# Optimization experiments

Hardware: AMD Instinct MI355X
Metric: run time of the kernel (lower is better)

Reference implementation:

```python
import jax, jax.numpy as jnp
import numpy as np

B, S, D_IN, HID, H = 4, 2048, 1024, 1024, 16
DH = HID // H


def setup_inputs() -> dict:
    key = jax.random.key(0)
    ks = jax.random.split(key, 10)
    s = 0.02
    return {
        "x": jax.random.normal(ks[0], (B, S, D_IN), dtype=jnp.float32),
        "Wq": jax.random.normal(ks[1], (D_IN, HID), dtype=jnp.float32) * s,
        "bq": jnp.zeros((HID,), dtype=jnp.float32),
        "Wk": jax.random.normal(ks[2], (D_IN, HID), dtype=jnp.float32) * s,
        "bk": jnp.zeros((HID,), dtype=jnp.float32),
        "Wv": jax.random.normal(ks[3], (D_IN, HID), dtype=jnp.float32) * s,
        "bv": jnp.zeros((HID,), dtype=jnp.float32),
        "Wo": jax.random.normal(ks[4], (HID, HID), dtype=jnp.float32) * s,
        "bo": jnp.zeros((HID,), dtype=jnp.float32),
        "padding_mask": jax.random.randint(ks[5], (B, S), 0, 2, dtype=jnp.int32),
    }


def reference(x, Wq, bq, Wk, bk, Wv, bv, Wo, bo, padding_mask):
    b, s, _ = x.shape
    q = (x @ Wq + bq).reshape(b, s, H, DH)  # [b, s, h, dh]
    k = (x @ Wk + bk).reshape(b, s, H, DH)
    v = (x @ Wv + bv).reshape(b, s, H, DH)

    # ALiBi: symmetric |i-j| distance bias, per-head slopes 2^{-m}
    r = jnp.arange(s)
    pos = jnp.abs(r[None, :] - r[:, None]).astype(jnp.float32)  # [s, s]
    step = 8.0 / H
    slopes = jnp.power(2.0, -jnp.arange(step, 8.0 + step, step, dtype=jnp.float32))  # [h]
    alibi = slopes[:, None, None] * pos[None, :, :]  # [h, s, s]

    scale = jnp.sqrt(jnp.float32(DH))
    attn = jnp.einsum("bqhd,bkhd->bhqk", q, k)
    attn = (attn - alibi[None]) / scale
    attn = jnp.where(padding_mask[:, None, None, :] == 0, -jnp.inf, attn)
    p = jax.nn.softmax(attn, axis=-1)

    out = jnp.einsum("bhqk,bkhd->bqhd", p, v).reshape(b, s, HID)
    return out @ Wo + bo
```

## Files before the change

kernel.cpp:

```cpp
#include <hip/hip_runtime.h>
#include <stdint.h>

#define NB     4
#define SEQ    2048
#define NH     16
#define DHD    64
#define DM     1024
#define MTOT   (NB*SEQ)
#define HSZ    (SEQ*DHD)

typedef __attribute__((ext_vector_type(8))) short bf16x8;
typedef __attribute__((ext_vector_type(4))) float f32x4;

__device__ __forceinline__ short f2bf(float f) {
  uint32_t u = __float_as_uint(f);
  u = (u + 0x7FFFu + ((u >> 16) & 1u)) >> 16;
  return (short)u;
}

__device__ __forceinline__ uint32_t cvtpk(float lo, float hi) {
  uint32_t r;
  asm("v_cvt_pk_bf16_f32 %0, %1, %2" : "=v"(r) : "v"(lo), "v"(hi));
  return r;
}

__device__ __forceinline__ float exp2a(float x) {
  float r;
  asm("v_exp_f32 %0, %1" : "=v"(r) : "v"(x));
  return r;
}

__device__ __forceinline__ float max3f(float a, float b, float c) {
  return fmaxf(fmaxf(a, b), c);
}

__device__ __forceinline__ f32x4 mfma16(bf16x8 a, bf16x8 b, f32x4 c) {
  return __builtin_amdgcn_mfma_f32_16x16x32_bf16(a, b, c, 0, 0, 0);
}

__device__ __forceinline__ void async16(const void* g, void* l) {
  __builtin_amdgcn_global_load_lds(
      (const __attribute__((address_space(1))) void*)g,
      (__attribute__((address_space(3))) void*)l, 16, 0, 0);
}

__global__ void k_cast(const float* __restrict__ in, short* __restrict__ out, int n) {
  int i = (blockIdx.x * blockDim.x + threadIdx.x) * 8;
  if (i >= n) return;
  float4 a = *reinterpret_cast<const float4*>(in + i);
  float4 b = *reinterpret_cast<const float4*>(in + i + 4);
  bf16x8 v;
  v[0] = f2bf(a.x); v[1] = f2bf(a.y); v[2] = f2bf(a.z); v[3] = f2bf(a.w);
  v[4] = f2bf(b.x); v[5] = f2bf(b.y); v[6] = f2bf(b.z); v[7] = f2bf(b.w);
  *reinterpret_cast<bf16x8*>(out + i) = v;
}

__global__ void k_maskbias(const int* __restrict__ pm, float* __restrict__ fb, int n) {
  int i = blockIdx.x * blockDim.x + threadIdx.x;
  if (i < n) fb[i] = pm[i] ? 0.0f : -1e30f;
}

__global__ void k_transpose4(const float* __restrict__ Wq, const float* __restrict__ Wk,
                             const float* __restrict__ Wv, const float* __restrict__ Wo,
                             short* __restrict__ wqkv, short* __restrict__ wot) {
  __shared__ float tile[32][33];
  int z = blockIdx.z;
  const float* in = (z == 0) ? Wq : (z == 1) ? Wk : (z == 2) ? Wv : Wo;
  short* out = (z < 3) ? (wqkv + (size_t)z * 1024 * DM) : wot;
  int n0 = blockIdx.x * 32, k0 = blockIdx.y * 32;
  int tx = threadIdx.x, ty = threadIdx.y;
  #pragma unroll
  for (int i = 0; i < 32; i += 8)
    tile[ty + i][tx] = in[(size_t)(k0 + ty + i) * DM + n0 + tx];
  __syncthreads();
  #pragma unroll
  for (int i = 0; i < 32; i += 8)
    out[(size_t)(n0 + ty + i) * DM + k0 + tx] = f2bf(tile[tx][ty + i]);
}

__global__ void __launch_bounds__(256) k_gemm_qkv(const short* __restrict__ A,
                                                  const short* __restrict__ Bt,
                                                  const float* __restrict__ bq,
                                                  const float* __restrict__ bk,
                                                  const float* __restrict__ bv,
                                                  short* __restrict__ Qo,
                                                  short* __restrict__ KF,
                                                  short* __restrict__ VF,
                                                  float qscale) {
  __shared__ short lA[128 * 32];
  __shared__ short lB[128 * 32];
  int lin = blockIdx.y * gridDim.x + blockIdx.x;
  int swz = (lin & 7) * 192 + (lin >> 3);
  int m0 = (swz & 63) * 128, n0 = (swz >> 6) * 128;
  int seg = n0 >> 10;
  const float* bias = (seg == 0) ? bq : (seg == 1) ? bk : bv;
  float scale = (seg == 0) ? qscale : 1.0f;
  int tid = threadIdx.x, lane = tid & 63, w = tid >> 6;
  int wr = w >> 1, wc = w & 1;
  int l15 = lane & 15, lg = lane >> 4;
  f32x4 acc[4][4] = {};

  int r0 = tid >> 2, c0 = (tid & 3) * 8;
  int r1 = (tid + 256) >> 2, c1 = ((tid + 256) & 3) * 8;
  const short* ga0 = A + (size_t)(m0 + r0) * DM + c0;
  const short* ga1 = A + (size_t)(m0 + r1) * DM + c1;
  const short* gb0 = Bt + (size_t)(n0 + r0) * DM + c0;
  const short* gb1 = Bt + (size_t)(n0 + r1) * DM + c1;
  short* lA0 = lA + w * 512;
  short* lA1 = lA + 2048 + w * 512;
  short* lB0 = lB + w * 512;
  short* lB1 = lB + 2048 + w * 512;

  for (int k0 = 0; k0 < DM; k0 += 32) {
    async16(ga0 + k0, lA0);
    async16(ga1 + k0, lA1);
    async16(gb0 + k0, lB0);
    async16(gb1 + k0, lB1);
    __syncthreads();
    bf16x8 af[4], bfr[4];
    #pragma unroll
    for (int i = 0; i < 4; ++i) {
      af[i]  = *reinterpret_cast<const bf16x8*>(lA + (wr * 64 + i * 16 + l15) * 32 + lg * 8);
      bfr[i] = *reinterpret_cast<const bf16x8*>(lB + (wc * 64 + i * 16 + l15) * 32 + lg * 8);
    }
    #pragma unroll
    for (int i = 0; i < 4; ++i)
      #pragma unroll
      for (int j = 0; j < 4; ++j)
        acc[i][j] = mfma16(af[i], bfr[j], acc[i][j]);
    __syncthreads();
  }

  #pragma unroll
  for (int j = 0; j < 4; ++j) {
    int cg = n0 + wc * 64 + j * 16 + l15;
    int cloc = cg & 1023;
    float bval = bias[cloc];
    #pragma unroll
    for (int i = 0; i < 4; ++i) {
      #pragma unroll
      for (int r = 0; r < 4; ++r) {
        int rg = m0 + wr * 64 + i * 16 + lg * 4 + r;
        float val = (acc[i][j][r] + bval) * scale;
        if (seg == 0) {
          Qo[(size_t)rg * DM + cloc] = f2bf(val);
        } else if (seg == 1) {
          int bh2 = ((rg >> 11) << 4) | (cloc >> 6);
          int dh = cloc & 63, sl = rg & 2047;
          size_t fi = (size_t)bh2 * HSZ + (size_t)(sl >> 4) * 1024
                    + (size_t)((((dh >> 3) * 16 + (sl & 15)) * 8) + (dh & 7));
          KF[fi] = f2bf(val);
        } else {
          int bh2 = ((rg >> 11) << 4) | (cloc >> 6);
          int dh = cloc & 63, sl = rg & 2047;
          size_t fi = (size_t)bh2 * HSZ + (size_t)(sl >> 6) * 4096
                    + (size_t)((((dh >> 4) * 8 + ((sl >> 3) & 7)) * 16 + (dh & 15)) * 8 + (sl & 7));
          VF[fi] = f2bf(val);
        }
      }
    }
  }
}

__global__ void __launch_bounds__(256) k_gemm_out(const short* __restrict__ A,
                                                  const short* __restrict__ Bt,
                                                  const float* __restrict__ bias,
                                                  float* __restrict__ C) {
  __shared__ short lA[128 * 32];
  __shared__ short lB[128 * 32];
  int lin = blockIdx.y * gridDim.x + blockIdx.x;
  int s = ((lin & 7) << 6) | (lin >> 3);
  int m0 = (s & 63) * 128, n0 = (s >> 6) * 128;
  int tid = threadIdx.x, lane = tid & 63, w = tid >> 6;
  int wr = w >> 1, wc = w & 1;
  int l15 = lane & 15, lg = lane >> 4;
  f32x4 acc[4][4] = {};

  int r0 = tid >> 2, c0 = (tid & 3) * 8;
  int r1 = (tid + 256) >> 2, c1 = ((tid + 256) & 3) * 8;
  const short* ga0 = A + (size_t)(m0 + r0) * DM + c0;
  const short* ga1 = A + (size_t)(m0 + r1) * DM + c1;
  const short* gb0 = Bt + (size_t)(n0 + r0) * DM + c0;
  const short* gb1 = Bt + (size_t)(n0 + r1) * DM + c1;
  short* lA0 = lA + w * 512;
  short* lA1 = lA + 2048 + w * 512;
  short* lB0 = lB + w * 512;
  short* lB1 = lB + 2048 + w * 512;

  for (int k0 = 0; k0 < DM; k0 += 32) {
    async16(ga0 + k0, lA0);
    async16(ga1 + k0, lA1);
    async16(gb0 + k0, lB0);
    async16(gb1 + k0, lB1);
    __syncthreads();
    bf16x8 af[4], bfr[4];
    #pragma unroll
    for (int i = 0; i < 4; ++i) {
      af[i]  = *reinterpret_cast<const bf16x8*>(lA + (wr * 64 + i * 16 + l15) * 32 + lg * 8);
      bfr[i] = *reinterpret_cast<const bf16x8*>(lB + (wc * 64 + i * 16 + l15) * 32 + lg * 8);
    }
    #pragma unroll
    for (int i = 0; i < 4; ++i)
      #pragma unroll
      for (int j = 0; j < 4; ++j)
        acc[i][j] = mfma16(af[i], bfr[j], acc[i][j]);
    __syncthreads();
  }

  #pragma unroll
  for (int j = 0; j < 4; ++j) {
    int cg = n0 + wc * 64 + j * 16 + l15;
    float bv = bias[cg];
    #pragma unroll
    for (int i = 0; i < 4; ++i) {
      #pragma unroll
      for (int r = 0; r < 4; ++r) {
        int rg = m0 + wr * 64 + i * 16 + lg * 4 + r;
        C[(size_t)rg * DM + cg] = acc[i][j][r] + bv;
      }
    }
  }
}

__device__ __forceinline__ void softmax_half(const f32x4* st, const float4* fb4,
                                             float c2, float d0, int lg,
                                             float& mrun, float& ssum,
                                             f32x4* acc, uint32_t* wb) {
  float l[16];
  #pragma unroll
  for (int t = 0; t < 4; ++t) {
    l[t * 4 + 0] = fmaf(-c2, fabsf(d0 - (float)(t * 16 + 0)), st[t][0] + fb4[t].x);
    l[t * 4 + 1] = fmaf(-c2, fabsf(d0 - (float)(t * 16 + 1)), st[t][1] + fb4[t].y);
    l[t * 4 + 2] = fmaf(-c2, fabsf(d0 - (float)(t * 16 + 2)), st[t][2] + fb4[t].z);
    l[t * 4 + 3] = fmaf(-c2, fabsf(d0 - (float)(t * 16 + 3)), st[t][3] + fb4[t].w);
  }
  float ma = max3f(l[0], l[1], l[2]);
  float mb = max3f(l[3], l[4], l[5]);
  float mc = max3f(l[6], l[7], l[8]);
  float md = max3f(l[9], l[10], l[11]);
  float me = max3f(l[12], l[13], l[14]);
  float tmax = fmaxf(max3f(ma, mb, mc), max3f(md, me, l[15]));

  if (!__all(tmax <= mrun + 8.0f)) {
    tmax = fmaxf(tmax, __shfl_xor(tmax, 16));
    tmax = fmaxf(tmax, __shfl_xor(tmax, 32));
    float mn = fmaxf(mrun, tmax);
    float fsc = exp2a(mrun - mn);
    mrun = mn;
    ssum *= fsc;
    #pragma unroll
    for (int td = 0; td < 4; ++td) acc[td] *= fsc;
  }

  float p[16];
  #pragma unroll
  for (int i = 0; i < 16; ++i) p[i] = exp2a(l[i] - mrun);
  float a0 = p[0] + p[1],  a1 = p[2] + p[3],  a2 = p[4] + p[5],  a3 = p[6] + p[7];
  float a4 = p[8] + p[9],  a5 = p[10] + p[11], a6 = p[12] + p[13], a7 = p[14] + p[15];
  float b0 = a0 + a1, b1 = a2 + a3, b2 = a4 + a5, b3 = a6 + a7;
  ssum += (b0 + b1) + (b2 + b3);

  #pragma unroll
  for (int t = 0; t < 4; ++t) {
    uint2 wv = { cvtpk(p[t * 4 + 0], p[t * 4 + 1]), cvtpk(p[t * 4 + 2], p[t * 4 + 3]) };
    *reinterpret_cast<uint2*>(wb + t * 8 + lg * 2) = wv;
  }
}

#define ISSUE_KA(DST, KT) do {                                              \
  const short* kp_ = kbase + (size_t)((KT) >> 4) * 1024;                    \
  _Pragma("unroll")                                                         \
  for (int t_ = 0; t_ < 4; ++t_) {                                          \
    DST[t_][0] = *reinterpret_cast<const bf16x8*>(kp_ + t_ * 1024);         \
    DST[t_][1] = *reinterpret_cast<const bf16x8*>(kp_ + t_ * 1024 + 512);   \
  }                                                                         \
} while (0)

#define TILE(KA, KAN, KT, PRE) do {                                         \
  float4 fb4[4];                                                            \
  _Pragma("unroll")                                                         \
  for (int t_ = 0; t_ < 4; ++t_)                                            \
    fb4[t_] = *reinterpret_cast<const float4*>(fb + (KT) + t_ * 16 + lg * 4);\
  const short* vp_ = vbase + (size_t)((KT) >> 6) * 4096;                    \
  bf16x8 va[4][2];                                                          \
  _Pragma("unroll")                                                         \
  for (int td_ = 0; td_ < 4; ++td_) {                                       \
    va[td_][0] = *reinterpret_cast<const bf16x8*>(vp_ + (td_ * 8 + 0) * 128);\
    va[td_][1] = *reinterpret_cast<const bf16x8*>(vp_ + (td_ * 8 + 4) * 128);\
  }                                                                         \
  if (PRE) { ISSUE_KA(KAN, (KT) + 64); }                                    \
  __builtin_amdgcn_sched_barrier(0);                                        \
  f32x4 stA[4], stB[4];                                                     \
  __builtin_amdgcn_s_setprio(1);                                            \
  _Pragma("unroll")                                                         \
  for (int t_ = 0; t_ < 4; ++t_) {                                          \
    f32x4 zA = {};                                                          \
    zA = mfma16(KA[t_][0], bqA0, zA);                                       \
    stA[t_] = mfma16(KA[t_][1], bqA1, zA);                                  \
    f32x4 zB = {};                                                          \
    zB = mfma16(KA[t_][0], bqB0, zB);                                       \
    stB[t_] = mfma16(KA[t_][1], bqB1, zB);                                  \
  }                                                                         \
  __builtin_amdgcn_s_setprio(0);                                            \
  softmax_half(stA, fb4, c2, d0A, lg, mrunA, ssumA, accA, wbA);             \
  softmax_half(stB, fb4, c2, d0B, lg, mrunB, ssumB, accB, wbB);             \
  asm volatile("s_waitcnt lgkmcnt(0)" ::: "memory");                        \
  __builtin_amdgcn_sched_barrier(0);                                        \
  __builtin_amdgcn_s_setprio(1);                                            \
  _Pragma("unroll")                                                         \
  for (int ks_ = 0; ks_ < 2; ++ks_) {                                       \
    int t_ = ks_ * 2 + (lg >> 1);                                           \
    bf16x8 pfA = *reinterpret_cast<const bf16x8*>(wbA + t_ * 8 + (lg & 1) * 4);\
    bf16x8 pfB = *reinterpret_cast<const bf16x8*>(wbB + t_ * 8 + (lg & 1) * 4);\
    _Pragma("unroll")                                                       \
    for (int td_ = 0; td_ < 4; ++td_) {                                     \
      accA[td_] = mfma16(va[td_][ks_], pfA, accA[td_]);                     \
      accB[td_] = mfma16(va[td_][ks_], pfB, accB[td_]);                     \
    }                                                                       \
  }                                                                         \
  __builtin_amdgcn_s_setprio(0);                                            \
  d0A -= 64.0f; d0B -= 64.0f;                                               \
} while (0)

__global__ void __launch_bounds__(64, 2) k_attn(const short* __restrict__ Q,
                                                const short* __restrict__ KF,
                                                const short* __restrict__ VF,
                                                const float* __restrict__ fbias,
                                                short* __restrict__ O) {
  __shared__ uint32_t pbuf[2 * 16 * 38];
  int g = blockIdx.x;
  int qb = (g >> 3) & 63;
  int bh = (g & 7) + ((g >> 9) << 3);
  int b = bh >> 4, h = bh & 15;
  int lane = threadIdx.x;
  int l15 = lane & 15, lg = lane >> 4;
  int q0 = qb * 32;
  float c2 = exp2f(-0.5f * (float)(h + 1)) * 0.125f * 1.44269504f;

  const short* qpA = Q + (size_t)(b * SEQ + q0 + l15) * DM + h * DHD + lg * 8;
  bf16x8 bqA0 = *reinterpret_cast<const bf16x8*>(qpA);
  bf16x8 bqA1 = *reinterpret_cast<const bf16x8*>(qpA + 32);
  const short* qpB = qpA + (size_t)16 * DM;
  bf16x8 bqB0 = *reinterpret_cast<const bf16x8*>(qpB);
  bf16x8 bqB1 = *reinterpret_cast<const bf16x8*>(qpB + 32);

  const short* kbase = KF + (size_t)bh * HSZ + lane * 8;
  const short* vbase = VF + (size_t)bh * HSZ + lane * 8;
  const float* fb = fbias + b * SEQ;
  uint32_t* wbA = pbuf + l15 * 38;
  uint32_t* wbB = pbuf + 608 + l15 * 38;

  float mrunA = 0.0f, ssumA = 0.0f, mrunB = 0.0f, ssumB = 0.0f;
  f32x4 accA[4] = {}, accB[4] = {};
  float d0A = (float)(q0 + l15) - (float)(lg * 4);
  float d0B = d0A + 16.0f;

  bf16x8 kaX[4][2], kaY[4][2];
  ISSUE_KA(kaX, 0);

  for (int kt = 0; kt < SEQ; kt += 128) {
    TILE(kaX, kaY, kt, true);
    TILE(kaY, kaX, kt + 64, (kt + 128) < SEQ);
  }

  ssumA += __shfl_xor(ssumA, 16);
  ssumA += __shfl_xor(ssumA, 32);
  ssumB += __shfl_xor(ssumB, 16);
  ssumB += __shfl_xor(ssumB, 32);

  float invA = 1.0f / ssumA;
  float invB = 1.0f / ssumB;
  short* opA = O + (size_t)(b * SEQ + q0 + l15) * DM + h * DHD;
  short* opB = opA + (size_t)16 * DM;
  #pragma unroll
  for (int td = 0; td < 4; ++td) {
    uint2 wvA = { cvtpk(accA[td][0] * invA, accA[td][1] * invA),
                  cvtpk(accA[td][2] * invA, accA[td][3] * invA) };
    *reinterpret_cast<uint2*>(opA + td * 16 + lg * 4) = wvA;
    uint2 wvB = { cvtpk(accB[td][0] * invB, accB[td][1] * invB),
                  cvtpk(accB[td][2] * invB, accB[td][3] * invB) };
    *reinterpret_cast<uint2*>(opB + td * 16 + lg * 4) = wvB;
  }
}

extern "C" void kernel_launch(void* const* d_in, const int* in_sizes, int n_in,
                              void* d_out, int out_size, void* d_ws, size_t ws_size,
                              hipStream_t stream) {
  const float* x  = (const float*)d_in[0];
  const float* Wq = (const float*)d_in[1];
  const float* bq = (const float*)d_in[2];
  const float* Wk = (const float*)d_in[3];
  const float* bk = (const float*)d_in[4];
  const float* Wv = (const float*)d_in[5];
  const float* bv = (const float*)d_in[6];
  const float* Wo = (const float*)d_in[7];
  const float* bo = (const float*)d_in[8];
  const int*   pm = (const int*)d_in[9];

  char* ws = (char*)d_ws;
  const size_t MB = 1ull << 20;
  short* xb   = (short*)(ws + 0 * MB);
  short* q    = (short*)(ws + 16 * MB);
  short* kf   = (short*)(ws + 32 * MB);
  short* vf   = (short*)(ws + 48 * MB);
  short* ob   = (short*)(ws + 64 * MB);
  short* wqkv = (short*)(ws + 80 * MB);
  short* wot  = (short*)(ws + 86 * MB);
  float* fbias = (float*)(ws + 88 * MB);

  k_cast<<<dim3(MTOT * DM / 8 / 256), dim3(256), 0, stream>>>(x, xb, MTOT * DM);
  k_maskbias<<<dim3(MTOT / 256), dim3(256), 0, stream>>>(pm, fbias, MTOT);
  k_transpose4<<<dim3(32, 32, 4), dim3(32, 8), 0, stream>>>(Wq, Wk, Wv, Wo, wqkv, wot);
  k_gemm_qkv<<<dim3(64, 24), dim3(256), 0, stream>>>(xb, wqkv, bq, bk, bv,
                                                     q, kf, vf, 0.125f * 1.44269504f);
  k_attn<<<dim3(SEQ / 32 * NB * NH), dim3(64), 0, stream>>>(q, kf, vf, fbias, ob);
  k_gemm_out<<<dim3(64, 8), dim3(256), 0, stream>>>(ob, wot, bo, (float*)d_out);
}
```

Measured before the change: 238.3 us.

## Software-pipeline attention PV matmul one tile behind softmax with double-buffered P and V

The P·V MFMA for each key tile is deferred to the next tile's iteration. It now overlaps with the next QK^T and softmax instead of waiting on the LDS writes of P right after they are issued. P is double-buffered in shared memory and V fragments are double-buffered in registers. When a running-max rescale is needed, the pending PV is flushed first so it uses the old scale, and a final PV drains the pipeline after the loop. This costs extra VGPRs and twice the LDS for P, which may pressure occupancy.

```diff
diff --git a/kernel.cpp b/kernel.cpp
--- a/kernel.cpp
+++ b/kernel.cpp
@@ -222,51 +222,6 @@
   }
 }
 
-__device__ __forceinline__ void softmax_half(const f32x4* st, const float4* fb4,
-                                             float c2, float d0, int lg,
-                                             float& mrun, float& ssum,
-                                             f32x4* acc, uint32_t* wb) {
-  float l[16];
-  #pragma unroll
-  for (int t = 0; t < 4; ++t) {
-    l[t * 4 + 0] = fmaf(-c2, fabsf(d0 - (float)(t * 16 + 0)), st[t][0] + fb4[t].x);
-    l[t * 4 + 1] = fmaf(-c2, fabsf(d0 - (float)(t * 16 + 1)), st[t][1] + fb4[t].y);
-    l[t * 4 + 2] = fmaf(-c2, fabsf(d0 - (float)(t * 16 + 2)), st[t][2] + fb4[t].z);
-    l[t * 4 + 3] = fmaf(-c2, fabsf(d0 - (float)(t * 16 + 3)), st[t][3] + fb4[t].w);
-  }
-  float ma = max3f(l[0], l[1], l[2]);
-  float mb = max3f(l[3], l[4], l[5]);
-  float mc = max3f(l[6], l[7], l[8]);
-  float md = max3f(l[9], l[10], l[11]);
-  float me = max3f(l[12], l[13], l[14]);
-  float tmax = fmaxf(max3f(ma, mb, mc), max3f(md, me, l[15]));
-
-  if (!__all(tmax <= mrun + 8.0f)) {
-    tmax = fmaxf(tmax, __shfl_xor(tmax, 16));
-    tmax = fmaxf(tmax, __shfl_xor(tmax, 32));
-    float mn = fmaxf(mrun, tmax);
-    float fsc = exp2a(mrun - mn);
-    mrun = mn;
-    ssum *= fsc;
-    #pragma unroll
-    for (int td = 0; td < 4; ++td) acc[td] *= fsc;
-  }
-
-  float p[16];
-  #pragma unroll
-  for (int i = 0; i < 16; ++i) p[i] = exp2a(l[i] - mrun);
-  float a0 = p[0] + p[1],  a1 = p[2] + p[3],  a2 = p[4] + p[5],  a3 = p[6] + p[7];
-  float a4 = p[8] + p[9],  a5 = p[10] + p[11], a6 = p[12] + p[13], a7 = p[14] + p[15];
-  float b0 = a0 + a1, b1 = a2 + a3, b2 = a4 + a5, b3 = a6 + a7;
-  ssum += (b0 + b1) + (b2 + b3);
-
-  #pragma unroll
-  for (int t = 0; t < 4; ++t) {
-    uint2 wv = { cvtpk(p[t * 4 + 0], p[t * 4 + 1]), cvtpk(p[t * 4 + 2], p[t * 4 + 3]) };
-    *reinterpret_cast<uint2*>(wb + t * 8 + lg * 2) = wv;
-  }
-}
-
 #define ISSUE_KA(DST, KT) do {                                              \
   const short* kp_ = kbase + (size_t)((KT) >> 4) * 1024;                    \
   _Pragma("unroll")                                                         \
@@ -276,17 +231,70 @@
   }                                                                         \
 } while (0)
 
-#define TILE(KA, KAN, KT, PRE) do {                                         \
+#define LOGITS(ST, FB4, D0, L, TMX) do {                                    \
+  _Pragma("unroll")                                                         \
+  for (int t_ = 0; t_ < 4; ++t_) {                                          \
+    L[t_ * 4 + 0] = fmaf(-c2, fabsf((D0) - (float)(t_ * 16 + 0)), ST[t_][0] + FB4[t_].x); \
+    L[t_ * 4 + 1] = fmaf(-c2, fabsf((D0) - (float)(t_ * 16 + 1)), ST[t_][1] + FB4[t_].y); \
+    L[t_ * 4 + 2] = fmaf(-c2, fabsf((D0) - (float)(t_ * 16 + 2)), ST[t_][2] + FB4[t_].z); \
+    L[t_ * 4 + 3] = fmaf(-c2, fabsf((D0) - (float)(t_ * 16 + 3)), ST[t_][3] + FB4[t_].w); \
+  }                                                                         \
+  float ma_ = max3f(L[0], L[1], L[2]);                                      \
+  float mb_ = max3f(L[3], L[4], L[5]);                                      \
+  float mc_ = max3f(L[6], L[7], L[8]);                                      \
+  float md_ = max3f(L[9], L[10], L[11]);                                    \
+  float me_ = max3f(L[12], L[13], L[14]);                                   \
+  TMX = fmaxf(max3f(ma_, mb_, mc_), max3f(md_, me_, L[15]));                \
+} while (0)
+
+#define RESCALE(TMX, MRUN, SSUM, ACC) do {                                  \
+  TMX = fmaxf(TMX, __shfl_xor(TMX, 16));                                    \
+  TMX = fmaxf(TMX, __shfl_xor(TMX, 32));                                    \
+  float mn_ = fmaxf(MRUN, TMX);                                             \
+  float fsc_ = exp2a(MRUN - mn_);                                           \
+  MRUN = mn_; SSUM *= fsc_;                                                 \
+  _Pragma("unroll")                                                         \
+  for (int td_ = 0; td_ < 4; ++td_) ACC[td_] *= fsc_;                       \
+} while (0)
+
+#define FINISH(L, MRUN, SSUM, WB) do {                                      \
+  float p_[16];                                                             \
+  _Pragma("unroll")                                                         \
+  for (int i_ = 0; i_ < 16; ++i_) p_[i_] = exp2a(L[i_] - MRUN);             \
+  float a0_ = p_[0] + p_[1],  a1_ = p_[2] + p_[3];                          \
+  float a2_ = p_[4] + p_[5],  a3_ = p_[6] + p_[7];                          \
+  float a4_ = p_[8] + p_[9],  a5_ = p_[10] + p_[11];                        \
+  float a6_ = p_[12] + p_[13], a7_ = p_[14] + p_[15];                       \
+  SSUM += ((a0_ + a1_) + (a2_ + a3_)) + ((a4_ + a5_) + (a6_ + a7_));        \
+  _Pragma("unroll")                                                         \
+  for (int t_ = 0; t_ < 4; ++t_) {                                          \
+    uint2 wv_ = { cvtpk(p_[t_ * 4 + 0], p_[t_ * 4 + 1]),                    \
+                  cvtpk(p_[t_ * 4 + 2], p_[t_ * 4 + 3]) };                  \
+    *reinterpret_cast<uint2*>((WB) + t_ * 8 + lg * 2) = wv_;                \
+  }                                                                         \
+} while (0)
+
+#define PVHALF(ACC, WBP, VAP) do {                                          \
+  _Pragma("unroll")                                                         \
+  for (int ks_ = 0; ks_ < 2; ++ks_) {                                       \
+    int t_ = ks_ * 2 + (lg >> 1);                                           \
+    bf16x8 pf_ = *reinterpret_cast<const bf16x8*>((WBP) + t_ * 8 + (lg & 1) * 4); \
+    _Pragma("unroll")                                                       \
+    for (int td_ = 0; td_ < 4; ++td_)                                       \
+      ACC[td_] = mfma16(VAP[td_][ks_], pf_, ACC[td_]);                      \
+  }                                                                         \
+} while (0)
+
+#define TILE(KA, KAN, VA, VAP, WBA, WBB, WBAP, WBBP, KT, PRE, PREV) do {    \
   float4 fb4[4];                                                            \
   _Pragma("unroll")                                                         \
   for (int t_ = 0; t_ < 4; ++t_)                                            \
     fb4[t_] = *reinterpret_cast<const float4*>(fb + (KT) + t_ * 16 + lg * 4);\
   const short* vp_ = vbase + (size_t)((KT) >> 6) * 4096;                    \
-  bf16x8 va[4][2];                                                          \
   _Pragma("unroll")                                                         \
   for (int td_ = 0; td_ < 4; ++td_) {                                       \
-    va[td_][0] = *reinterpret_cast<const bf16x8*>(vp_ + (td_ * 8 + 0) * 128);\
-    va[td_][1] = *reinterpret_cast<const bf16x8*>(vp_ + (td_ * 8 + 4) * 128);\
+    VA[td_][0] = *reinterpret_cast<const bf16x8*>(vp_ + (td_ * 8 + 0) * 128);\
+    VA[td_][1] = *reinterpret_cast<const bf16x8*>(vp_ + (td_ * 8 + 4) * 128);\
   }                                                                         \
   if (PRE) { ISSUE_KA(KAN, (KT) + 64); }                                    \
   __builtin_amdgcn_sched_barrier(0);                                        \
@@ -302,22 +310,23 @@
     stB[t_] = mfma16(KA[t_][1], bqB1, zB);                                  \
   }                                                                         \
   __builtin_amdgcn_s_setprio(0);                                            \
-  softmax_half(stA, fb4, c2, d0A, lg, mrunA, ssumA, accA, wbA);             \
-  softmax_half(stB, fb4, c2, d0B, lg, mrunB, ssumB, accB, wbB);             \
-  asm volatile("s_waitcnt lgkmcnt(0)" ::: "memory");                        \
-  __builtin_amdgcn_sched_barrier(0);                                        \
+  float lA_[16], lB_[16], tmA_, tmB_;                                       \
+  LOGITS(stA, fb4, d0A, lA_, tmA_);                                         \
+  LOGITS(stB, fb4, d0B, lB_, tmB_);                                         \
+  bool pvA_ = false, pvB_ = false;                                          \
+  if (!__all(tmA_ <= mrunA + 8.0f)) {                                       \
+    if (PREV) { PVHALF(accA, WBAP, VAP); pvA_ = true; }                     \
+    RESCALE(tmA_, mrunA, ssumA, accA);                                      \
+  }                                                                         \
+  if (!__all(tmB_ <= mrunB + 8.0f)) {                                       \
+    if (PREV) { PVHALF(accB, WBBP, VAP); pvB_ = true; }                     \
+    RESCALE(tmB_, mrunB, ssumB, accB);                                      \
+  }                                                                         \
+  FINISH(lA_, mrunA, ssumA, WBA);                                           \
+  FINISH(lB_, mrunB, ssumB, WBB);                                           \
   __builtin_amdgcn_s_setprio(1);                                            \
-  _Pragma("unroll")                                                         \
-  for (int ks_ = 0; ks_ < 2; ++ks_) {                                       \
-    int t_ = ks_ * 2 + (lg >> 1);                                           \
-    bf16x8 pfA = *reinterpret_cast<const bf16x8*>(wbA + t_ * 8 + (lg & 1) * 4);\
-    bf16x8 pfB = *reinterpret_cast<const bf16x8*>(wbB + t_ * 8 + (lg & 1) * 4);\
-    _Pragma("unroll")                                                       \
-    for (int td_ = 0; td_ < 4; ++td_) {                                     \
-      accA[td_] = mfma16(va[td_][ks_], pfA, accA[td_]);                     \
-      accB[td_] = mfma16(va[td_][ks_], pfB, accB[td_]);                     \
-    }                                                                       \
-  }                                                                         \
+  if ((PREV) && !pvA_) PVHALF(accA, WBAP, VAP);                             \
+  if ((PREV) && !pvB_) PVHALF(accB, WBBP, VAP);                             \
   __builtin_amdgcn_s_setprio(0);                                            \
   d0A -= 64.0f; d0B -= 64.0f;                                               \
 } while (0)
@@ -327,7 +336,7 @@
                                                 const short* __restrict__ VF,
                                                 const float* __restrict__ fbias,
                                                 short* __restrict__ O) {
-  __shared__ uint32_t pbuf[2 * 16 * 38];
+  __shared__ uint32_t pbuf[4 * 16 * 38];
   int g = blockIdx.x;
   int qb = (g >> 3) & 63;
   int bh = (g & 7) + ((g >> 9) << 3);
@@ -347,21 +356,29 @@
   const short* kbase = KF + (size_t)bh * HSZ + lane * 8;
   const short* vbase = VF + (size_t)bh * HSZ + lane * 8;
   const float* fb = fbias + b * SEQ;
-  uint32_t* wbA = pbuf + l15 * 38;
-  uint32_t* wbB = pbuf + 608 + l15 * 38;
+  uint32_t* wbA0 = pbuf + l15 * 38;
+  uint32_t* wbB0 = pbuf + 608 + l15 * 38;
+  uint32_t* wbA1 = pbuf + 1216 + l15 * 38;
+  uint32_t* wbB1 = pbuf + 1824 + l15 * 38;
 
   float mrunA = 0.0f, ssumA = 0.0f, mrunB = 0.0f, ssumB = 0.0f;
   f32x4 accA[4] = {}, accB[4] = {};
   float d0A = (float)(q0 + l15) - (float)(lg * 4);
   float d0B = d0A + 16.0f;
 
-  bf16x8 kaX[4][2], kaY[4][2];
+  bf16x8 kaX[4][2], kaY[4][2], vaX[4][2], vaY[4][2];
   ISSUE_KA(kaX, 0);
 
-  for (int kt = 0; kt < SEQ; kt += 128) {
-    TILE(kaX, kaY, kt, true);
-    TILE(kaY, kaX, kt + 64, (kt + 128) < SEQ);
-  }
+  TILE(kaX, kaY, vaX, vaY, wbA0, wbB0, wbA1, wbB1, 0, true, false);
+  TILE(kaY, kaX, vaY, vaX, wbA1, wbB1, wbA0, wbB0, 64, true, true);
+  for (int kt = 128; kt < SEQ; kt += 128) {
+    TILE(kaX, kaY, vaX, vaY, wbA0, wbB0, wbA1, wbB1, kt, true, true);
+    TILE(kaY, kaX, vaY, vaX, wbA1, wbB1, wbA0, wbB0, kt + 64, (kt + 128) < SEQ, true);
+  }
+  __builtin_amdgcn_s_setprio(1);
+  PVHALF(accA, wbA1, vaY);
+  PVHALF(accB, wbB1, vaY);
+  __builtin_amdgcn_s_setprio(0);
 
   ssumA += __shfl_xor(ssumA, 16);
   ssumA += __shfl_xor(ssumA, 32);
```

Result: no change. 240.2 us (+0.8%).
